# Performance work log

Hardware: AMD Instinct MI355X
Metric: run time of the kernel (lower is better)

Reference implementation:

```python
import jax, jax.numpy as jnp
import numpy as np
import math

DIM = 512
HEADS = 8
DH = DIM // HEADS
B, C, H, W = 2, 512, 48, 48


def setup_inputs() -> dict:
    key = jax.random.key(0)
    k1, k2, k3, k4 = jax.random.split(key, 4)
    x = jax.random.normal(k1, (B, C, H, W), dtype=jnp.float32)
    # torch Linear weights: [out_features, in_features]
    w_qkv = jax.random.normal(k2, (3 * DIM, DIM), dtype=jnp.float32) * (DIM ** -0.5)
    w_out = jax.random.normal(k3, (DIM, DIM), dtype=jnp.float32) * (DIM ** -0.5)
    b_out = jax.random.normal(k4, (DIM,), dtype=jnp.float32) * 0.01
    wavelength = jnp.asarray(0.1, dtype=jnp.float32)
    return {"x": x, "w_qkv": w_qkv, "w_out": w_out, "b_out": b_out, "wavelength": wavelength}


def reference(x, w_qkv, w_out, b_out, wavelength):
    b, c, h, w = x.shape
    n = h * w
    scale = DH ** -0.5

    x_flat = x.reshape(b, c, n).transpose(0, 2, 1)  # [B, N, C]
    qkv = jnp.einsum('bnc,dc->bnd', x_flat, w_qkv)   # [B, N, 3*DIM]
    q, k, v = jnp.split(qkv, 3, axis=-1)

    def to_heads(t):
        return t.reshape(b, n, HEADS, DH).transpose(0, 2, 1, 3)  # [B, h, N, dh]

    q, k, v = to_heads(q), to_heads(k), to_heads(v)

    dots = jnp.einsum('bhid,bhjd->bhij', q, k) * scale  # [B, h, N, N]

    # Fresnel interference bias over spatial positions
    yy, xx = jnp.meshgrid(jnp.arange(h), jnp.arange(w), indexing='ij')
    positions = jnp.stack([yy, xx], axis=-1).astype(jnp.float32).reshape(-1, 2)  # [N, 2]
    pos_diff = positions[None, :, :] - positions[:, None, :]  # [N, N, 2]
    distances = jnp.sqrt(jnp.sum(pos_diff ** 2, axis=-1) + 1e-8)  # [N, N]
    phase = 2.0 * math.pi * distances / (jnp.abs(wavelength) * h + 1e-6)
    interference = jnp.cos(phase)

    dots = dots + interference[None, None, :, :] * 0.1
    attn = jax.nn.softmax(dots, axis=-1)
    out = jnp.einsum('bhij,bhjd->bhid', attn, v)  # [B, h, N, dh]
    out = out.transpose(0, 2, 1, 3).reshape(b, n, HEADS * DH)  # [B, N, DIM]
    out = jnp.einsum('bnd,od->bno', out, w_out) + b_out
    return out.transpose(0, 2, 1).reshape(b, c, h, w)
```

## Files before the change

kernel.cpp:

```cpp
#include <hip/hip_runtime.h>
#include <math.h>

#define BB 2
#define CC 512
#define NN 2304
#define NH 8
#define DD 512
#define D3 1536
#define WIDTH 48
#define C1 0.18033688f
#define NSPLIT 2
#define KTILES 18

typedef _Float16 h8 __attribute__((ext_vector_type(8)));
typedef _Float16 h4 __attribute__((ext_vector_type(4)));
typedef _Float16 h2 __attribute__((ext_vector_type(2)));
typedef float f4 __attribute__((ext_vector_type(4)));

__device__ __forceinline__ void gload16(const void* g, void* s) {
  __builtin_amdgcn_global_load_lds(
      (const __attribute__((address_space(1))) unsigned int*)g,
      (__attribute__((address_space(3))) unsigned int*)s, 16, 0, 0);
}

__global__ __launch_bounds__(256) void prep_k(
    const float* __restrict__ x, const float* __restrict__ wq,
    const float* __restrict__ wo, const float* __restrict__ wavp,
    _Float16* __restrict__ btf, _Float16* __restrict__ xt,
    _Float16* __restrict__ wqh, _Float16* __restrict__ woh)
{
  __shared__ float Ls[32][33];
  const int t = threadIdx.x;
  const int bx = blockIdx.x;
  const int job = blockIdx.y;

  if (job == 0) {
    if (bx >= 648) return;
    const int gid = bx * 256 + t;
    const int tile = gid >> 7, tid = gid & 127;
    const int qbk = tile / 36, ktk = tile % 36;
    const int w = tid >> 6, quad = (tid >> 4) & 3, l15 = tid & 15;
    const float pc = 6.283185307179586f / (fabsf(wavp[0]) * (float)WIDTH + 1e-6f);
    _Float16* o = btf + (((size_t)qbk * 36 + ktk) * 128 + tid) * 32;
#pragma unroll
    for (int g = 0; g < 4; ++g) {
      h8 v;
#pragma unroll
      for (int e = 0; e < 8; ++e) {
        const int j = g * 8 + e;
        const int nt = j >> 4, mt = (j >> 2) & 3, r = j & 3;
        const int q = qbk * 64 + w * 32 + nt * 16 + l15;
        const int k = ktk * 64 + mt * 16 + quad * 4 + r;
        const float dy = (float)(q / WIDTH) - (float)(k / WIDTH);
        const float dx = (float)(q % WIDTH) - (float)(k % WIDTH);
        const float dist = sqrtf(dy * dy + dx * dx + 1e-8f);
        v[e] = (_Float16)(0.1f * __cosf(dist * pc) * 1.44269504f);
      }
      *(h8*)(o + g * 8) = v;
    }
  } else if (job == 1) {
    const int b = bx / 1152, rem = bx % 1152;
    const int c0 = (rem / 72) * 32, n0 = (rem % 72) * 32;
#pragma unroll
    for (int p = 0; p < 4; ++p) {
      const int cl = (t >> 5) + p * 8, nl = t & 31;
      Ls[cl][nl] = x[((size_t)b * CC + c0 + cl) * NN + n0 + nl];
    }
    __syncthreads();
#pragma unroll
    for (int p = 0; p < 2; ++p) {
      const int nl = (t >> 4) + p * 16, cl = (t & 15) * 2;
      h2 v = {(_Float16)Ls[cl][nl], (_Float16)Ls[cl + 1][nl]};
      *(h2*)(xt + ((size_t)b * NN + n0 + nl) * CC + c0 + cl) = v;
    }
  } else {
    if (bx >= 1024) return;
    const int idx = bx * 256 + t;
    const int NQ = (D3 * CC) / 4;
    if (idx < NQ) {
      float4 v = *(const float4*)(wq + (size_t)idx * 4);
      h4 o = {(_Float16)v.x, (_Float16)v.y, (_Float16)v.z, (_Float16)v.w};
      *(h4*)(wqh + (size_t)idx * 4) = o;
    } else {
      const int j = idx - NQ;
      float4 v = *(const float4*)(wo + (size_t)j * 4);
      h4 o = {(_Float16)v.x, (_Float16)v.y, (_Float16)v.z, (_Float16)v.w};
      *(h4*)(woh + (size_t)j * 4) = o;
    }
  }
}

__global__ __launch_bounds__(128) void qkv_gemm_k(
    const _Float16* __restrict__ xt, const _Float16* __restrict__ wqh,
    _Float16* __restrict__ qb, _Float16* __restrict__ kb,
    _Float16* __restrict__ vb)
{
  __shared__ _Float16 Xs[2][128][32];
  __shared__ _Float16 Ws[2][64][32];
  const int t = threadIdx.x;
  const int lane = t & 63, w = t >> 6;
  const int l15 = lane & 15, quad = lane >> 4;
  const int n0 = blockIdx.x * 128;
  const int d0 = blockIdx.y * 64;
  const int b  = blockIdx.z;
  const bool isv = (d0 >= 2 * DD);
  const _Float16* xb = xt + (size_t)b * NN * CC;
  const int lrow = lane >> 2, lcol = (lane & 3) * 8;

  f4 acc[4][4];
#pragma unroll
  for (int mt = 0; mt < 4; ++mt)
#pragma unroll
    for (int nt = 0; nt < 4; ++nt) acc[mt][nt] = (f4)(0.f);

  auto stage = [&](int bf, int c0) {
#pragma unroll
    for (int k = 0; k < 4; ++k) {
      const int row = w * 64 + k * 16 + lrow;
      gload16(xb + (size_t)(n0 + row) * CC + c0 + lcol,
              &Xs[bf][w * 64 + k * 16][0]);
    }
#pragma unroll
    for (int k = 0; k < 2; ++k) {
      const int row = w * 32 + k * 16 + lrow;
      gload16(wqh + (size_t)(d0 + row) * CC + c0 + lcol,
              &Ws[bf][w * 32 + k * 16][0]);
    }
  };

  stage(0, 0);
  for (int i = 0; i < 16; ++i) {
    const int cur = i & 1;
    __syncthreads();
    if (i < 15) stage(cur ^ 1, (i + 1) * 32);
    h8 wfr[4], xfr[4];
#pragma unroll
    for (int mt = 0; mt < 4; ++mt)
      wfr[mt] = *(const h8*)&Ws[cur][mt * 16 + l15][quad * 8];
#pragma unroll
    for (int nt = 0; nt < 4; ++nt)
      xfr[nt] = *(const h8*)&Xs[cur][w * 64 + nt * 16 + l15][quad * 8];
    if (!isv) {
#pragma unroll
      for (int mt = 0; mt < 4; ++mt)
#pragma unroll
        for (int nt = 0; nt < 4; ++nt)
          acc[mt][nt] = __builtin_amdgcn_mfma_f32_16x16x32_f16(
              wfr[mt], xfr[nt], acc[mt][nt], 0, 0, 0);
    } else {
#pragma unroll
      for (int mt = 0; mt < 4; ++mt)
#pragma unroll
        for (int nt = 0; nt < 4; ++nt)
          acc[mt][nt] = __builtin_amdgcn_mfma_f32_16x16x32_f16(
              xfr[nt], wfr[mt], acc[mt][nt], 0, 0, 0);
    }
  }

  if (!isv) {
    const int which = d0 >> 9;
    _Float16* buf = which == 0 ? qb : kb;
    const int h = (d0 & 511) >> 6;
#pragma unroll
    for (int mt = 0; mt < 4; ++mt) {
      const int dh = mt * 16 + quad * 4;
#pragma unroll
      for (int nt = 0; nt < 4; ++nt) {
        const int token = n0 + w * 64 + nt * 16 + l15;
        h4 o = {(_Float16)acc[mt][nt][0], (_Float16)acc[mt][nt][1],
                (_Float16)acc[mt][nt][2], (_Float16)acc[mt][nt][3]};
        *(h4*)(buf + (((size_t)b * NH + h) * NN + token) * 64 + dh) = o;
      }
    }
  } else {
    const int h = (d0 - 2 * DD) >> 6;
#pragma unroll
    for (int mt = 0; mt < 4; ++mt) {
      const int dh = mt * 16 + l15;
#pragma unroll
      for (int nt = 0; nt < 4; ++nt) {
        const int token = n0 + w * 64 + nt * 16 + quad * 4;
        h4 o = {(_Float16)acc[mt][nt][0], (_Float16)acc[mt][nt][1],
                (_Float16)acc[mt][nt][2], (_Float16)acc[mt][nt][3]};
        *(h4*)(vb + (((size_t)b * NH + h) * 64 + dh) * NN + token) = o;
      }
    }
  }
}

__global__ __launch_bounds__(128, 3) void attn_k(
    const _Float16* __restrict__ qb, const _Float16* __restrict__ kb,
    const _Float16* __restrict__ vb, const _Float16* __restrict__ btf,
    _Float16* __restrict__ op, float* __restrict__ lp)
{
  __shared__ _Float16 Ks[64][72];
  __shared__ _Float16 Vs[64][72];
  __shared__ _Float16 Ps[2][32][72];

  const int t    = threadIdx.x;
  const int lane = t & 63;
  const int w    = t >> 6;
  const int l15  = lane & 15;
  const int quad = lane >> 4;
  const int qt = blockIdx.x >> 1;
  const int s  = blockIdx.x & 1;
  const int h = blockIdx.y, b = blockIdx.z;
  const int n0 = qt * 64;
  const size_t base = ((size_t)b * NH + h) * NN * 64;
  const _Float16* qp = qb + base;
  const _Float16* kp = kb + base;
  const _Float16* vp = vb + base;

  h8 qf[2][2];
#pragma unroll
  for (int nt = 0; nt < 2; ++nt)
#pragma unroll
    for (int ks = 0; ks < 2; ++ks)
      qf[nt][ks] = *(const h8*)(qp + (size_t)(n0 + w * 32 + nt * 16 + l15) * 64 +
                                ks * 32 + quad * 8);

  f4 oc[4][2];
#pragma unroll
  for (int mt = 0; mt < 4; ++mt)
#pragma unroll
    for (int nt = 0; nt < 2; ++nt) oc[mt][nt] = (f4)(0.f);
  float lacc[2][4] = {};

  const int srow = t >> 3, soff = (t & 7) * 8;
  const _Float16* bp = btf + (((size_t)qt * 36 + s * KTILES) * 128 + t) * 32;

  for (int kt = 0; kt < KTILES; ++kt) {
    const int k0 = (s * KTILES + kt) * 64;
    h8 kr[4], vr[4], br[4];
#pragma unroll
    for (int r = 0; r < 4; ++r) {
      const int row = srow + r * 16;
      kr[r] = *(const h8*)(kp + (size_t)(k0 + row) * 64 + soff);
      vr[r] = *(const h8*)(vp + (size_t)row * NN + k0 + soff);
      br[r] = *(const h8*)(bp + r * 8);
    }
    bp += 128 * 32;
    __syncthreads();
#pragma unroll
    for (int r = 0; r < 4; ++r) {
      const int row = srow + r * 16;
      *(h8*)&Ks[row][soff] = kr[r];
      *(h8*)&Vs[row][soff] = vr[r];
    }
    __syncthreads();

    f4 st[4][2];
#pragma unroll
    for (int mt = 0; mt < 4; ++mt)
#pragma unroll
      for (int nt = 0; nt < 2; ++nt) st[mt][nt] = (f4)(0.f);
#pragma unroll
    for (int ks = 0; ks < 2; ++ks)
#pragma unroll
      for (int mt = 0; mt < 4; ++mt) {
        h8 kf = *(const h8*)&Ks[mt * 16 + l15][ks * 32 + quad * 8];
#pragma unroll
        for (int nt = 0; nt < 2; ++nt)
          st[mt][nt] = __builtin_amdgcn_mfma_f32_16x16x32_f16(
              kf, qf[nt][ks], st[mt][nt], 0, 0, 0);
      }

#pragma unroll
    for (int nt = 0; nt < 2; ++nt) {
      const int q = nt * 16 + l15;
#pragma unroll
      for (int mt = 0; mt < 4; ++mt) {
        h4 pk;
#pragma unroll
        for (int r = 0; r < 4; ++r) {
          const int j = nt * 16 + mt * 4 + r;
          const float bias = (float)br[j >> 3][j & 7];
          const float p = __builtin_exp2f(st[mt][nt][r] * C1 + bias);
          lacc[nt][r] += p;
          pk[r] = (_Float16)p;
        }
        *(h4*)&Ps[w][q][mt * 16 + quad * 4] = pk;
      }
    }

#pragma unroll
    for (int ks = 0; ks < 2; ++ks) {
      h8 pf[2];
#pragma unroll
      for (int nt = 0; nt < 2; ++nt)
        pf[nt] = *(const h8*)&Ps[w][nt * 16 + l15][ks * 32 + quad * 8];
#pragma unroll
      for (int mt = 0; mt < 4; ++mt) {
        h8 vf = *(const h8*)&Vs[mt * 16 + l15][ks * 32 + quad * 8];
#pragma unroll
        for (int nt = 0; nt < 2; ++nt)
          oc[mt][nt] = __builtin_amdgcn_mfma_f32_16x16x32_f16(
              vf, pf[nt], oc[mt][nt], 0, 0, 0);
      }
    }
  }

#pragma unroll
  for (int nt = 0; nt < 2; ++nt) {
    float l = lacc[nt][0] + lacc[nt][1] + lacc[nt][2] + lacc[nt][3];
    l += __shfl_xor(l, 16);
    l += __shfl_xor(l, 32);
    const float inv = 1.f / l;
    const int qi = n0 + w * 32 + nt * 16 + l15;
    _Float16* od = op + (size_t)s * BB * NN * DD +
                   ((size_t)b * NN + qi) * DD + h * 64;
#pragma unroll
    for (int mt = 0; mt < 4; ++mt) {
      const int dh = mt * 16 + quad * 4;
      h4 o = {(_Float16)(oc[mt][nt][0] * inv), (_Float16)(oc[mt][nt][1] * inv),
              (_Float16)(oc[mt][nt][2] * inv), (_Float16)(oc[mt][nt][3] * inv)};
      *(h4*)(od + dh) = o;
    }
    if (quad == 0)
      lp[(size_t)s * BB * NH * NN + ((size_t)b * NH + h) * NN + qi] = l;
  }
}

__global__ __launch_bounds__(64) void outcomb_k(
    const _Float16* __restrict__ op, const float* __restrict__ lp,
    const _Float16* __restrict__ woh, const float* __restrict__ bias,
    float* __restrict__ out)
{
  __shared__ _Float16 Hs[64][32];
  __shared__ _Float16 Ws2[2][64][32];
  const int t = threadIdx.x;
  const int l15 = t & 15, quad = t >> 4;
  const int n0 = blockIdx.x * 64;
  const int o0 = blockIdx.y * 64;
  const int b  = blockIdx.z;
  const int lrow = t >> 2, lcol = (t & 3) * 8;
  const size_t SZO = (size_t)BB * NN * DD;
  const size_t SZL = (size_t)BB * NH * NN;

  f4 acc[4][4];
#pragma unroll
  for (int mt = 0; mt < 4; ++mt)
#pragma unroll
    for (int nt = 0; nt < 4; ++nt) acc[mt][nt] = (f4)(0.f);

  auto stage_w = [&](int bf, int c0) {
#pragma unroll
    for (int k = 0; k < 4; ++k)
      gload16(woh + (size_t)(o0 + k * 16 + lrow) * DD + c0 + lcol,
              &Ws2[bf][k * 16][0]);
  };

  stage_w(0, 0);
  for (int i = 0; i < 16; ++i) {
    const int cur = i & 1;
    const int c0 = i * 32;
    const int h = c0 >> 6;
    h8 a[4];
#pragma unroll
    for (int k = 0; k < 4; ++k) {
      const int row = n0 + k * 16 + lrow;
      const float l0 = lp[((size_t)b * NH + h) * NN + row];
      const float l1 = lp[SZL + ((size_t)b * NH + h) * NN + row];
      const float inv = 1.f / (l0 + l1);
      const float w0 = l0 * inv, w1 = l1 * inv;
      const size_t off = ((size_t)b * NN + row) * DD + c0 + lcol;
      h8 o0v = *(const h8*)(op + off);
      h8 o1v = *(const h8*)(op + SZO + off);
#pragma unroll
      for (int e = 0; e < 8; ++e)
        a[k][e] = (_Float16)((float)o0v[e] * w0 + (float)o1v[e] * w1);
    }
    __syncthreads();
#pragma unroll
    for (int k = 0; k < 4; ++k)
      *(h8*)&Hs[k * 16 + lrow][lcol] = a[k];
    if (i < 15) stage_w(cur ^ 1, c0 + 32);
    __syncthreads();

    h8 hf[4], wf[4];
#pragma unroll
    for (int mt = 0; mt < 4; ++mt)
      hf[mt] = *(const h8*)&Hs[mt * 16 + l15][quad * 8];
#pragma unroll
    for (int nt = 0; nt < 4; ++nt)
      wf[nt] = *(const h8*)&Ws2[cur][nt * 16 + l15][quad * 8];
#pragma unroll
    for (int mt = 0; mt < 4; ++mt)
#pragma unroll
      for (int nt = 0; nt < 4; ++nt)
        acc[mt][nt] = __builtin_amdgcn_mfma_f32_16x16x32_f16(
            hf[mt], wf[nt], acc[mt][nt], 0, 0, 0);
  }

#pragma unroll
  for (int nt = 0; nt < 4; ++nt) {
    const int o = o0 + nt * 16 + l15;
    const float bv = bias[o];
#pragma unroll
    for (int mt = 0; mt < 4; ++mt) {
      const int token = n0 + mt * 16 + quad * 4;
      float4 v = {acc[mt][nt][0] + bv, acc[mt][nt][1] + bv,
                  acc[mt][nt][2] + bv, acc[mt][nt][3] + bv};
      *(float4*)(out + ((size_t)b * DD + o) * NN + token) = v;
    }
  }
}

extern "C" void kernel_launch(void* const* d_in, const int* in_sizes, int n_in,
                              void* d_out, int out_size, void* d_ws, size_t ws_size,
                              hipStream_t stream)
{
  (void)in_sizes; (void)n_in; (void)out_size; (void)ws_size;
  const float* x     = (const float*)d_in[0];
  const float* w_qkv = (const float*)d_in[1];
  const float* w_out = (const float*)d_in[2];
  const float* b_out = (const float*)d_in[3];
  const float* wav   = (const float*)d_in[4];
  float* out = (float*)d_out;

  const size_t SZ  = (size_t)BB * NH * NN * 64;
  const size_t BTF = (size_t)36 * 36 * 128 * 32;

  _Float16* qb  = (_Float16*)d_ws;
  _Float16* kb  = qb + SZ;
  _Float16* vb  = kb + SZ;
  _Float16* btf = vb + SZ;
  _Float16* op  = btf + BTF;
  float*    lpf = (float*)(op + 2 * SZ);
  _Float16* woh = (_Float16*)(lpf + 2 * (size_t)BB * NH * NN);
  _Float16* xt  = op;
  _Float16* wqh = op + SZ;

  prep_k    <<<dim3(2304, 3), 256, 0, stream>>>(x, w_qkv, w_out, wav,
                                                btf, xt, wqh, woh);
  qkv_gemm_k<<<dim3(NN / 128, D3 / 64, BB), 128, 0, stream>>>(xt, wqh, qb, kb, vb);
  attn_k    <<<dim3(NN / 64 * NSPLIT, NH, BB), 128, 0, stream>>>(
                 qb, kb, vb, btf, op, lpf);
  outcomb_k <<<dim3(NN / 64, DD / 64, BB), 64, 0, stream>>>(
                 op, lpf, woh, b_out, out);
}
```

Before: 170.2 us.

## Share K/V tiles across 128 queries per block and add 4-way KV split

The attention kernel now uses 256-thread blocks covering 128 queries (two 64-query subgroups), so each staged K/V tile is reused by twice as many queries and per-thread staging loads are halved. The KV sequence split becomes runtime-selectable, using 4 splits when the workspace is large enough, which keeps the grid size up despite the larger blocks. The output-combine kernel is templated on the split count and prefetches the next partial outputs and row sums one iteration ahead to overlap loads with the MFMA work. More splits mean more partial-output traffic and combine work, and the larger blocks raise register and LDS pressure per CU.

```diff
diff --git a/kernel.cpp b/kernel.cpp
--- a/kernel.cpp
+++ b/kernel.cpp
@@ -9,8 +9,6 @@
 #define D3 1536
 #define WIDTH 48
 #define C1 0.18033688f
-#define NSPLIT 2
-#define KTILES 18
 
 typedef _Float16 h8 __attribute__((ext_vector_type(8)));
 typedef _Float16 h4 __attribute__((ext_vector_type(4)));
@@ -188,24 +186,28 @@
   }
 }
 
-__global__ __launch_bounds__(128, 3) void attn_k(
+__global__ __launch_bounds__(256, 4) void attn_k(
     const _Float16* __restrict__ qb, const _Float16* __restrict__ kb,
     const _Float16* __restrict__ vb, const _Float16* __restrict__ btf,
-    _Float16* __restrict__ op, float* __restrict__ lp)
+    _Float16* __restrict__ op, float* __restrict__ lp,
+    int slog, int ktiles)
 {
   __shared__ _Float16 Ks[64][72];
   __shared__ _Float16 Vs[64][72];
-  __shared__ _Float16 Ps[2][32][72];
+  __shared__ _Float16 Ps[4][32][72];
 
   const int t    = threadIdx.x;
   const int lane = t & 63;
   const int w    = t >> 6;
   const int l15  = lane & 15;
   const int quad = lane >> 4;
-  const int qt = blockIdx.x >> 1;
-  const int s  = blockIdx.x & 1;
+  const int qsub = w >> 1;
+  const int wp   = w & 1;
+  const int qt   = blockIdx.x >> slog;
+  const int s    = blockIdx.x & ((1 << slog) - 1);
   const int h = blockIdx.y, b = blockIdx.z;
-  const int n0 = qt * 64;
+  const int qt64 = qt * 2 + qsub;
+  const int qbase = qt64 * 64 + wp * 32;
   const size_t base = ((size_t)b * NH + h) * NN * 64;
   const _Float16* qp = qb + base;
   const _Float16* kp = kb + base;
@@ -216,7 +218,7 @@
   for (int nt = 0; nt < 2; ++nt)
 #pragma unroll
     for (int ks = 0; ks < 2; ++ks)
-      qf[nt][ks] = *(const h8*)(qp + (size_t)(n0 + w * 32 + nt * 16 + l15) * 64 +
+      qf[nt][ks] = *(const h8*)(qp + (size_t)(qbase + nt * 16 + l15) * 64 +
                                 ks * 32 + quad * 8);
 
   f4 oc[4][2];
@@ -226,26 +228,29 @@
     for (int nt = 0; nt < 2; ++nt) oc[mt][nt] = (f4)(0.f);
   float lacc[2][4] = {};
 
-  const int srow = t >> 3, soff = (t & 7) * 8;
-  const _Float16* bp = btf + (((size_t)qt * 36 + s * KTILES) * 128 + t) * 32;
-
-  for (int kt = 0; kt < KTILES; ++kt) {
-    const int k0 = (s * KTILES + kt) * 64;
-    h8 kr[4], vr[4], br[4];
-#pragma unroll
-    for (int r = 0; r < 4; ++r) {
-      const int row = srow + r * 16;
-      kr[r] = *(const h8*)(kp + (size_t)(k0 + row) * 64 + soff);
-      vr[r] = *(const h8*)(vp + (size_t)row * NN + k0 + soff);
-      br[r] = *(const h8*)(bp + r * 8);
-    }
+  const int sr = t >> 3, so = (t & 7) * 8;
+  const int tid128 = wp * 64 + lane;
+  const _Float16* bp =
+      btf + (((size_t)qt64 * 36 + s * ktiles) * 128 + tid128) * 32;
+
+  for (int kt = 0; kt < ktiles; ++kt) {
+    const int k0 = (s * ktiles + kt) * 64;
+    h8 kr[2], vr[2], br[4];
+#pragma unroll
+    for (int r = 0; r < 2; ++r) {
+      const int row = sr + r * 32;
+      kr[r] = *(const h8*)(kp + (size_t)(k0 + row) * 64 + so);
+      vr[r] = *(const h8*)(vp + (size_t)row * NN + k0 + so);
+    }
+#pragma unroll
+    for (int r = 0; r < 4; ++r) br[r] = *(const h8*)(bp + r * 8);
     bp += 128 * 32;
     __syncthreads();
 #pragma unroll
-    for (int r = 0; r < 4; ++r) {
-      const int row = srow + r * 16;
-      *(h8*)&Ks[row][soff] = kr[r];
-      *(h8*)&Vs[row][soff] = vr[r];
+    for (int r = 0; r < 2; ++r) {
+      const int row = sr + r * 32;
+      *(h8*)&Ks[row][so] = kr[r];
+      *(h8*)&Vs[row][so] = vr[r];
     }
     __syncthreads();
 
@@ -306,7 +311,7 @@
     l += __shfl_xor(l, 16);
     l += __shfl_xor(l, 32);
     const float inv = 1.f / l;
-    const int qi = n0 + w * 32 + nt * 16 + l15;
+    const int qi = qbase + nt * 16 + l15;
     _Float16* od = op + (size_t)s * BB * NN * DD +
                    ((size_t)b * NN + qi) * DD + h * 64;
 #pragma unroll
@@ -321,6 +326,7 @@
   }
 }
 
+template <int NS>
 __global__ __launch_bounds__(64) void outcomb_k(
     const _Float16* __restrict__ op, const float* __restrict__ lp,
     const _Float16* __restrict__ woh, const float* __restrict__ bias,
@@ -350,33 +356,48 @@
               &Ws2[bf][k * 16][0]);
   };
 
+  float lv[4][NS];
+  h8 ov[4][NS];
+  auto load_raw = [&](int i) {
+    const int c0 = i * 32, h = c0 >> 6;
+#pragma unroll
+    for (int k = 0; k < 4; ++k) {
+      const int row = n0 + k * 16 + lrow;
+      const size_t off = ((size_t)b * NN + row) * DD + c0 + lcol;
+#pragma unroll
+      for (int s = 0; s < NS; ++s) {
+        lv[k][s] = lp[s * SZL + ((size_t)b * NH + h) * NN + row];
+        ov[k][s] = *(const h8*)(op + s * SZO + off);
+      }
+    }
+  };
+
   stage_w(0, 0);
+  load_raw(0);
   for (int i = 0; i < 16; ++i) {
     const int cur = i & 1;
-    const int c0 = i * 32;
-    const int h = c0 >> 6;
-    h8 a[4];
+    __syncthreads();
+    if (i < 15) stage_w(cur ^ 1, (i + 1) * 32);
 #pragma unroll
     for (int k = 0; k < 4; ++k) {
-      const int row = n0 + k * 16 + lrow;
-      const float l0 = lp[((size_t)b * NH + h) * NN + row];
-      const float l1 = lp[SZL + ((size_t)b * NH + h) * NN + row];
-      const float inv = 1.f / (l0 + l1);
-      const float w0 = l0 * inv, w1 = l1 * inv;
-      const size_t off = ((size_t)b * NN + row) * DD + c0 + lcol;
-      h8 o0v = *(const h8*)(op + off);
-      h8 o1v = *(const h8*)(op + SZO + off);
-#pragma unroll
-      for (int e = 0; e < 8; ++e)
-        a[k][e] = (_Float16)((float)o0v[e] * w0 + (float)o1v[e] * w1);
-    }
-    __syncthreads();
-#pragma unroll
-    for (int k = 0; k < 4; ++k)
-      *(h8*)&Hs[k * 16 + lrow][lcol] = a[k];
-    if (i < 15) stage_w(cur ^ 1, c0 + 32);
-    __syncthreads();
-
+      float tot = 0.f;
+#pragma unroll
+      for (int s = 0; s < NS; ++s) tot += lv[k][s];
+      const float inv = 1.f / tot;
+      float wgt[NS];
+#pragma unroll
+      for (int s = 0; s < NS; ++s) wgt[s] = lv[k][s] * inv;
+      h8 a;
+#pragma unroll
+      for (int e = 0; e < 8; ++e) {
+        float v = 0.f;
+#pragma unroll
+        for (int s = 0; s < NS; ++s) v += (float)ov[k][s][e] * wgt[s];
+        a[e] = (_Float16)v;
+      }
+      *(h8*)&Hs[k * 16 + lrow][lcol] = a;
+    }
+    if (i < 15) load_raw(i + 1);
     h8 hf[4], wf[4];
 #pragma unroll
     for (int mt = 0; mt < 4; ++mt)
@@ -410,7 +431,7 @@
                               void* d_out, int out_size, void* d_ws, size_t ws_size,
                               hipStream_t stream)
 {
-  (void)in_sizes; (void)n_in; (void)out_size; (void)ws_size;
+  (void)in_sizes; (void)n_in; (void)out_size;
   const float* x     = (const float*)d_in[0];
   const float* w_qkv = (const float*)d_in[1];
   const float* w_out = (const float*)d_in[2];
@@ -421,21 +442,31 @@
   const size_t SZ  = (size_t)BB * NH * NN * 64;
   const size_t BTF = (size_t)36 * 36 * 128 * 32;
 
+  const size_t need4 = 3 * SZ * 2 + BTF * 2 + 4 * SZ * 2 +
+                       4 * (size_t)BB * NH * NN * 4 + (size_t)DD * DD * 2;
+  const int nsplit = (ws_size >= need4) ? 4 : 2;
+  const int slog   = (nsplit == 4) ? 2 : 1;
+  const int ktiles = 36 / nsplit;
+
   _Float16* qb  = (_Float16*)d_ws;
   _Float16* kb  = qb + SZ;
   _Float16* vb  = kb + SZ;
   _Float16* btf = vb + SZ;
   _Float16* op  = btf + BTF;
-  float*    lpf = (float*)(op + 2 * SZ);
-  _Float16* woh = (_Float16*)(lpf + 2 * (size_t)BB * NH * NN);
+  float*    lpf = (float*)(op + (size_t)nsplit * SZ);
+  _Float16* woh = (_Float16*)(lpf + (size_t)nsplit * BB * NH * NN);
   _Float16* xt  = op;
   _Float16* wqh = op + SZ;
 
   prep_k    <<<dim3(2304, 3), 256, 0, stream>>>(x, w_qkv, w_out, wav,
                                                 btf, xt, wqh, woh);
   qkv_gemm_k<<<dim3(NN / 128, D3 / 64, BB), 128, 0, stream>>>(xt, wqh, qb, kb, vb);
-  attn_k    <<<dim3(NN / 64 * NSPLIT, NH, BB), 128, 0, stream>>>(
-                 qb, kb, vb, btf, op, lpf);
-  outcomb_k <<<dim3(NN / 64, DD / 64, BB), 64, 0, stream>>>(
-                 op, lpf, woh, b_out, out);
-}
+  attn_k    <<<dim3((NN / 128) * nsplit, NH, BB), 256, 0, stream>>>(
+                 qb, kb, vb, btf, op, lpf, slog, ktiles);
+  if (nsplit == 4)
+    outcomb_k<4><<<dim3(NN / 64, DD / 64, BB), 64, 0, stream>>>(
+                   op, lpf, woh, b_out, out);
+  else
+    outcomb_k<2><<<dim3(NN / 64, DD / 64, BB), 64, 0, stream>>>(
+                   op, lpf, woh, b_out, out);
+}
```

Result: slower. 183.3 us (+7.7%).
